# Performance work log

Measured on AMD Instinct MI355X. Metric: run time of the kernel, lower is better.

Reference implementation:

```python
import jax, jax.numpy as jnp
import numpy as np

D = 512       # d_model
M = 64        # working memory_dim
SE = 32       # episodic slots
SS = 64       # semantic slots
H = 4         # episodic heads
B, L = 2, 1024
BOT = max(D // 4, 32)  # controller bottleneck = 128


def _layernorm(x, g, b, eps=1e-5):
    mu = jnp.mean(x, axis=-1, keepdims=True)
    var = jnp.var(x, axis=-1, keepdims=True)
    return (x - mu) * jax.lax.rsqrt(var + eps) * g + b


def setup_inputs() -> dict:
    key = jax.random.key(0)
    ks = jax.random.split(key, 24)
    r = lambda i, shape, s=0.02: jax.random.normal(ks[i], shape, dtype=jnp.float32) * s
    return {
        "x": jax.random.normal(ks[0], (B, L, D), dtype=jnp.float32),
        # WorkingMemory (weights stored as (in, out))
        "Wq": r(1, (D, M)), "Wk": r(2, (D, M)), "Wv": r(3, (D, D)),
        "Wf": r(4, (D, M)), "bf": jnp.zeros((M,), jnp.float32),
        "Wo": r(5, (D, D)),
        "ln_g": jnp.ones((D,), jnp.float32), "ln_b": jnp.zeros((D,), jnp.float32),
        # EpisodicMemory
        "eslots": r(6, (1, SE, D)),
        "Eq": r(7, (D, D)), "Ek": r(8, (D, D)), "Ev": r(9, (D, D)), "Eo": r(10, (D, D)),
        # SemanticMemory
        "know": r(11, (1, SS, D)),
        "Sin": r(12, (D, D)),
        "Sg_w": r(13, (D, D)), "Sg_b": jnp.zeros((D,), jnp.float32),
        "So": r(14, (D, D)),
        # MemoryController
        "C1w": r(15, (D, BOT)), "C1b": jnp.zeros((BOT,), jnp.float32),
        "C2w": r(16, (BOT, 3)), "C2b": jnp.zeros((3,), jnp.float32),
    }


def _forward(x, Wq, Wk, Wv, Wf, bf, Wo, ln_g, ln_b,
             eslots, Eq, Ek, Ev, Eo,
             know, Sin, Sg_w, Sg_b, So,
             C1w, C1b, C2w, C2b):
    b, l, d = x.shape
    # ---- WorkingMemory (parallel gated linear attention) ----
    scale = M ** -0.5
    q = (jax.nn.elu(x @ Wq) + 1.0) * scale          # (B,L,M)
    k = jax.nn.elu(x @ Wk) + 1.0                    # (B,L,M)
    v = x @ Wv                                      # (B,L,D)
    forget = jax.nn.sigmoid(x @ Wf + bf)            # (B,L,M)
    log_f_cum = jnp.clip(jnp.cumsum(jnp.log(jnp.clip(forget, 1e-6, None)), axis=1), -20.0, 20.0)
    exp_neg = jnp.exp(-log_f_cum)
    exp_pos = jnp.exp(log_f_cum)
    kv = k[..., :, None] * v[..., None, :]          # (B,L,M,D) outer product
    cum_kv = jnp.cumsum(exp_neg[..., None] * kv, axis=1)
    Mstate = exp_pos[..., None] * cum_kv            # (B,L,M,D)
    z = exp_pos * jnp.cumsum(exp_neg * k, axis=1)   # (B,L,M)
    num = jnp.einsum('blm,blmd->bld', q, Mstate)
    den = jnp.einsum('blm,blm->bl', q, z)[..., None] + 1e-6
    w_out = _layernorm(num / den, ln_g, ln_b) @ Wo  # (B,L,D)

    # ---- EpisodicMemory (cross-attn to learned slots) ----
    hd = D // H
    mem = jnp.broadcast_to(eslots, (b, SE, D))
    qh = (x @ Eq).reshape(b, l, H, hd)
    kh = (mem @ Ek).reshape(b, SE, H, hd)
    vh = (mem @ Ev).reshape(b, SE, H, hd)
    scores = jnp.einsum('blhe,bshe->bhls', qh, kh) / jnp.sqrt(jnp.float32(hd))
    attn = jax.nn.softmax(scores, axis=-1)
    e_out = jnp.einsum('bhls,bshe->blhe', attn, vh).reshape(b, l, D) @ Eo

    # ---- SemanticMemory (single-head attn to knowledge, gated residual) ----
    kb = jnp.broadcast_to(know, (b, SS, D))
    qs = x @ Sin                                    # (B,L,D)
    s_scores = jnp.einsum('bld,bsd->bls', qs, kb) / jnp.sqrt(jnp.float32(D))
    s_attn = jax.nn.softmax(s_scores, axis=-1)
    retrieved = jnp.einsum('bls,bsd->bld', s_attn, kb)
    gate = jax.nn.sigmoid(x @ Sg_w + Sg_b)
    s_out = (gate * retrieved + (1.0 - gate) * x) @ So

    # ---- Controller fusion ----
    wts = jax.nn.softmax(jax.nn.silu(x @ C1w + C1b) @ C2w + C2b, axis=-1)  # (B,L,3)
    fused = (wts[..., 0:1] * w_out + wts[..., 1:2] * e_out + wts[..., 2:3] * s_out)
    return fused


def reference(x, Wq, Wk, Wv, Wf, bf, Wo, ln_g, ln_b,
              eslots, Eq, Ek, Ev, Eo,
              know, Sin, Sg_w, Sg_b, So,
              C1w, C1b, C2w, C2b):
    return _forward(x, Wq, Wk, Wv, Wf, bf, Wo, ln_g, ln_b,
                    eslots, Eq, Ek, Ev, Eo,
                    know, Sin, Sg_w, Sg_b, So,
                    C1w, C1b, C2w, C2b)
```

## Files before the change

### kernel.cpp

```cpp
#include <hip/hip_runtime.h>
#include <cstdint>

typedef unsigned int uint;
typedef unsigned short ushort;
typedef __attribute__((ext_vector_type(8))) short bf16x8;
typedef __attribute__((ext_vector_type(4))) float f32x4;

__device__ __forceinline__ ushort f2b(float f) {
  union { float f; uint u; } v; v.f = f;
  uint u = v.u;
  uint r = (u + 0x7FFFu + ((u >> 16) & 1u)) >> 16;
  return (ushort)r;
}
__device__ __forceinline__ float b2f(ushort h) {
  union { uint u; float f; } v; v.u = ((uint)h) << 16; return v.f;
}

__global__ __launch_bounds__(256) void k_prep(
    const float* __restrict__ x, const float* __restrict__ Wv, const float* __restrict__ Sg,
    const float* __restrict__ C1w, const float* __restrict__ Wq, const float* __restrict__ Wk,
    const float* __restrict__ Wo, const float* __restrict__ So, const float* __restrict__ know,
    const float* __restrict__ eslots, const float* __restrict__ Ek, const float* __restrict__ Ev,
    const float* __restrict__ Sin, const float* __restrict__ Wf, const float* __restrict__ bfb,
    ushort* __restrict__ X16, ushort* __restrict__ Wcat, ushort* __restrict__ Wfin,
    ushort* __restrict__ know16, float* __restrict__ kh, float* __restrict__ vh,
    float* __restrict__ logfb)
{
  __shared__ __align__(16) float pool[8320];
  int bid = blockIdx.x;
  int tid = threadIdx.x;
  int lane = tid & 63, wv = tid >> 6;

  if (bid < 128) {
    float* xS = pool;
    int r0 = bid * 16;
    #pragma unroll
    for (int it = 0; it < 8; ++it) {
      int p = it * 256 + tid;
      int rr = p >> 7, c4 = (p & 127) * 4;
      float4 v = *(const float4*)&x[(size_t)(r0 + rr) * 512 + c4];
      *(float4*)&xS[rr * 512 + c4] = v;
      uint2 o;
      o.x = (uint)f2b(v.x) | ((uint)f2b(v.y) << 16);
      o.y = (uint)f2b(v.z) | ((uint)f2b(v.w) << 16);
      *(uint2*)&X16[(size_t)(r0 + rr) * 512 + c4] = o;
    }
    __syncthreads();
    int row = tid >> 4, c4 = (tid & 15) * 4;
    float a0 = 0.f, a1 = 0.f, a2 = 0.f, a3 = 0.f;
    #pragma unroll 16
    for (int d = 0; d < 512; ++d) {
      float a = xS[row * 512 + d];
      float4 w = *(const float4*)&Wf[(size_t)d * 64 + c4];
      a0 += a * w.x; a1 += a * w.y; a2 += a * w.z; a3 += a * w.w;
    }
    float accs[4] = {a0, a1, a2, a3};
    #pragma unroll
    for (int j = 0; j < 4; ++j) {
      float logit = accs[j] + bfb[c4 + j];
      float s = 1.f / (1.f + expf(-logit));
      logfb[(size_t)(r0 + row) * 64 + c4 + j] = logf(fmaxf(s, 1e-6f));
    }
    return;
  }
  if (bid < 256) {
    int k = (bid - 128) * 4 + wv;
    const float* sp = Sin + (size_t)k * 512 + lane * 8;
    float4 s1 = *(const float4*)&sp[0];
    float4 s2 = *(const float4*)&sp[4];
    #pragma unroll 4
    for (int s = 0; s < 64; ++s) {
      const float* kp = know + (size_t)s * 512 + lane * 8;
      float4 k1 = *(const float4*)&kp[0];
      float4 k2 = *(const float4*)&kp[4];
      float part = s1.x * k1.x + s1.y * k1.y + s1.z * k1.z + s1.w * k1.w
                 + s2.x * k2.x + s2.y * k2.y + s2.z * k2.z + s2.w * k2.w;
      #pragma unroll
      for (int o = 32; o; o >>= 1) part += __shfl_xor(part, o);
      if (lane == 0) Wcat[(640 + s) * 512 + k] = f2b(part * 0.04419417382415922f);
    }
    return;
  }
  if (bid < 384) {
    int t = (bid - 256) * 256 + tid;
    int isv = (t >= 16384);
    int o = t & 16383; int s = o >> 9, j = o & 511;
    const float* W = isv ? Ev : Ek;
    const float* es = eslots + (size_t)s * 512;
    float a0 = 0.f, a1 = 0.f, a2 = 0.f, a3 = 0.f;
    #pragma unroll 8
    for (int d = 0; d < 512; d += 4) {
      a0 += es[d + 0] * W[(size_t)(d + 0) * 512 + j];
      a1 += es[d + 1] * W[(size_t)(d + 1) * 512 + j];
      a2 += es[d + 2] * W[(size_t)(d + 2) * 512 + j];
      a3 += es[d + 3] * W[(size_t)(d + 3) * 512 + j];
    }
    float acc = (a0 + a1) + (a2 + a3);
    (isv ? vh : kh)[(size_t)s * 512 + j] = acc;
    return;
  }
  if (bid < 672) {
    #define Tm(a,b) pool[(a) * 65 + (b)]
    int tt = bid - 384;
    const float* src; ushort* dst; int sld, dld, Nt, drow, dcol;
    if (tt < 64)       {           src = Wv;  dst = Wcat; sld = 512; dld = 512;  Nt = 8; drow = 0;    dcol = 0;   }
    else if (tt < 128) { tt -= 64; src = Sg;  dst = Wcat; sld = 512; dld = 512;  Nt = 8; drow = 704;  dcol = 0;   }
    else if (tt < 144) { tt -= 128; src = C1w; dst = Wcat; sld = 128; dld = 512; Nt = 2; drow = 1216; dcol = 0;   }
    else if (tt < 152) { tt -= 144; src = Wq;  dst = Wcat; sld = 64;  dld = 512; Nt = 1; drow = 1344; dcol = 0;   }
    else if (tt < 160) { tt -= 152; src = Wk;  dst = Wcat; sld = 64;  dld = 512; Nt = 1; drow = 1408; dcol = 0;   }
    else if (tt < 224) { tt -= 160; src = Wo;  dst = Wfin; sld = 512; dld = 1152; Nt = 8; drow = 0;   dcol = 0;   }
    else               { tt -= 224; src = So;  dst = Wfin; sld = 512; dld = 1152; Nt = 8; drow = 0;   dcol = 512; }
    int tk = tt / Nt, tn = tt % Nt;
    int k0 = tk * 64, n0 = tn * 64;
    int r = tid >> 4, c = (tid & 15) * 4;
    #pragma unroll
    for (int p = 0; p < 4; ++p) {
      int kk = p * 16 + r;
      float4 v = *(const float4*)&src[(size_t)(k0 + kk) * sld + n0 + c];
      Tm(c + 0, kk) = v.x; Tm(c + 1, kk) = v.y; Tm(c + 2, kk) = v.z; Tm(c + 3, kk) = v.w;
    }
    __syncthreads();
    int n = tid >> 2, kc = (tid & 3) * 16;
    uint u[8];
    #pragma unroll
    for (int j = 0; j < 8; ++j) {
      ushort lo = f2b(Tm(n, kc + 2 * j));
      ushort hi = f2b(Tm(n, kc + 2 * j + 1));
      u[j] = (uint)lo | ((uint)hi << 16);
    }
    size_t off = (size_t)(drow + n0 + n) * dld + dcol + k0 + kc;
    uint4 o1; o1.x = u[0]; o1.y = u[1]; o1.z = u[2]; o1.w = u[3];
    uint4 o2; o2.x = u[4]; o2.y = u[5]; o2.z = u[6]; o2.w = u[7];
    *(uint4*)&dst[off] = o1;
    *(uint4*)&dst[off + 8] = o2;
    #undef Tm
    return;
  }
  {
    int t = (bid - 672) * 256 + tid;
    #pragma unroll
    for (int j = 0; j < 2; ++j) {
      float4 v = *(const float4*)&know[(size_t)t * 8 + j * 4];
      uint2 o;
      o.x = (uint)f2b(v.x) | ((uint)f2b(v.y) << 16);
      o.y = (uint)f2b(v.z) | ((uint)f2b(v.w) << 16);
      *(uint2*)&know16[(size_t)t * 8 + j * 4] = o;
    }
  }
}

__global__ __launch_bounds__(256) void k_pre2(
    const float* __restrict__ Eq, const float* __restrict__ kh, const float* __restrict__ vh,
    const float* __restrict__ Eo, ushort* __restrict__ Wcat, ushort* __restrict__ Wfin)
{
  int bid = blockIdx.x;
  int tid = threadIdx.x;
  int lane = tid & 63, wv = tid >> 6;
  if (bid < 256) {
    int gw = bid * 4 + wv;
    #pragma unroll
    for (int pp = 0; pp < 2; ++pp) {
      int pair = gw * 2 + pp;
      int k = pair >> 2, h = pair & 3;
      const float* ep = Eq + (size_t)k * 512 + h * 128 + lane * 2;
      float e0 = ep[0], e1 = ep[1];
      #pragma unroll 4
      for (int s = 0; s < 32; ++s) {
        const float* kp = kh + (size_t)s * 512 + h * 128 + lane * 2;
        float part = e0 * kp[0] + e1 * kp[1];
        #pragma unroll
        for (int o = 32; o; o >>= 1) part += __shfl_xor(part, o);
        if (lane == 0) Wcat[(512 + h * 32 + s) * 512 + k] = f2b(part * 0.08838834764831845f);
      }
    }
  } else {
    int o = (bid - 256) * 256 + tid;
    int hs = o >> 9, j = o & 511;
    int h = hs >> 5, s = hs & 31;
    const float* vhp = vh + (size_t)s * 512 + h * 128;
    float acc = 0.f;
    #pragma unroll 16
    for (int e = 0; e < 128; ++e) acc += vhp[e] * Eo[(size_t)(h * 128 + e) * 512 + j];
    Wfin[(size_t)j * 1152 + 1024 + hs] = f2b(acc);
  }
}

__global__ __launch_bounds__(256) void k_gemm1(
    const ushort* __restrict__ A, const ushort* __restrict__ Bw, float* __restrict__ C,
    const float* __restrict__ sgb, const float* __restrict__ c1b)
{
  __shared__ __align__(16) ushort As[64 * 32];
  __shared__ __align__(16) ushort Bs[128 * 32];
  int tid = threadIdx.x;
  int lane = tid & 63, wv = tid >> 6;
  int wm = (wv & 1) * 32, wn = (wv >> 1) * 64;
  int lr = lane & 15, lk = lane >> 4;
  int m0 = blockIdx.y * 64, n0 = blockIdx.x * 128;
  f32x4 zero4 = {0.f, 0.f, 0.f, 0.f};
  f32x4 acc[2][4];
  #pragma unroll
  for (int a = 0; a < 2; ++a)
    #pragma unroll
    for (int b = 0; b < 4; ++b) acc[a][b] = zero4;
  for (int kt = 0; kt < 16; ++kt) {
    int k0 = kt * 32;
    {
      int p = tid, row = p >> 2, cc = p & 3;
      int cs = cc ^ ((row >> 1) & 3);
      *(uint4*)&As[p * 8] = *(const uint4*)&A[(size_t)(m0 + row) * 512 + k0 + cs * 8];
    }
    #pragma unroll
    for (int i = 0; i < 2; ++i) {
      int p = i * 256 + tid, row = p >> 2, cc = p & 3;
      int cs = cc ^ ((row >> 1) & 3);
      *(uint4*)&Bs[p * 8] = *(const uint4*)&Bw[(size_t)(n0 + row) * 512 + k0 + cs * 8];
    }
    __syncthreads();
    bf16x8 af[2], bfv[4];
    #pragma unroll
    for (int mi = 0; mi < 2; ++mi) {
      int row = wm + mi * 16 + lr;
      int cc = lk ^ ((row >> 1) & 3);
      af[mi] = *(bf16x8*)&As[row * 32 + cc * 8];
    }
    #pragma unroll
    for (int ni = 0; ni < 4; ++ni) {
      int row = wn + ni * 16 + lr;
      int cc = lk ^ ((row >> 1) & 3);
      bfv[ni] = *(bf16x8*)&Bs[row * 32 + cc * 8];
    }
    #pragma unroll
    for (int mi = 0; mi < 2; ++mi)
      #pragma unroll
      for (int ni = 0; ni < 4; ++ni)
        acc[mi][ni] = __builtin_amdgcn_mfma_f32_16x16x32_bf16(af[mi], bfv[ni], acc[mi][ni], 0, 0, 0);
    __syncthreads();
  }
  #pragma unroll
  for (int mi = 0; mi < 2; ++mi) {
    #pragma unroll
    for (int ni = 0; ni < 4; ++ni) {
      int col = n0 + wn + ni * 16 + lr;
      #pragma unroll
      for (int r = 0; r < 4; ++r) {
        int rowb = m0 + wm + mi * 16 + lk * 4 + r;
        float v = acc[mi][ni][r];
        if (col >= 704) {
          if (col < 1216) { v = 1.f / (1.f + __expf(-(v + sgb[col - 704]))); }
          else if (col < 1344) { float tt = v + c1b[col - 1216]; v = tt / (1.f + __expf(-tt)); }
          else if (col < 1408) { float e = (v > 0.f) ? v : (__expf(v) - 1.f); v = (e + 1.f) * 0.125f; }
          else if (col < 1472) { float e = (v > 0.f) ? v : (__expf(v) - 1.f); v = e + 1.f; }
        }
        C[(size_t)rowb * 1536 + col] = v;
      }
    }
  }
}

__global__ __launch_bounds__(256) void k_gemm2(
    const ushort* __restrict__ A, const ushort* __restrict__ Bw, float* __restrict__ C)
{
  __shared__ __align__(16) ushort As[64 * 32];
  __shared__ __align__(16) ushort Bs[64 * 32];
  int tid = threadIdx.x;
  int lane = tid & 63, wv = tid >> 6;
  int wm = (wv & 1) * 32, wn = (wv >> 1) * 32;
  int lr = lane & 15, lk = lane >> 4;
  int m0 = blockIdx.y * 64, n0 = blockIdx.x * 64;
  f32x4 zero4 = {0.f, 0.f, 0.f, 0.f};
  f32x4 acc[2][2];
  #pragma unroll
  for (int a = 0; a < 2; ++a)
    #pragma unroll
    for (int b = 0; b < 2; ++b) acc[a][b] = zero4;
  for (int kt = 0; kt < 36; ++kt) {
    int k0 = kt * 32;
    {
      int p = tid, row = p >> 2, cc = p & 3;
      int cs = cc ^ ((row >> 1) & 3);
      *(uint4*)&As[p * 8] = *(const uint4*)&A[(size_t)(m0 + row) * 1152 + k0 + cs * 8];
      *(uint4*)&Bs[p * 8] = *(const uint4*)&Bw[(size_t)(n0 + row) * 1152 + k0 + cs * 8];
    }
    __syncthreads();
    bf16x8 af[2], bfv[2];
    #pragma unroll
    for (int mi = 0; mi < 2; ++mi) {
      int row = wm + mi * 16 + lr;
      int cc = lk ^ ((row >> 1) & 3);
      af[mi] = *(bf16x8*)&As[row * 32 + cc * 8];
    }
    #pragma unroll
    for (int ni = 0; ni < 2; ++ni) {
      int row = wn + ni * 16 + lr;
      int cc = lk ^ ((row >> 1) & 3);
      bfv[ni] = *(bf16x8*)&Bs[row * 32 + cc * 8];
    }
    #pragma unroll
    for (int mi = 0; mi < 2; ++mi)
      #pragma unroll
      for (int ni = 0; ni < 2; ++ni)
        acc[mi][ni] = __builtin_amdgcn_mfma_f32_16x16x32_bf16(af[mi], bfv[ni], acc[mi][ni], 0, 0, 0);
    __syncthreads();
  }
  #pragma unroll
  for (int mi = 0; mi < 2; ++mi) {
    #pragma unroll
    for (int ni = 0; ni < 2; ++ni) {
      int col = n0 + wn + ni * 16 + lr;
      #pragma unroll
      for (int r = 0; r < 4; ++r) {
        int rowb = m0 + wm + mi * 16 + lk * 4 + r;
        C[(size_t)rowb * 512 + col] = acc[mi][ni][r];
      }
    }
  }
}

__global__ __launch_bounds__(256) void k_gatescan(
    const float* __restrict__ logfb, const float* __restrict__ P,
    float* __restrict__ cn, float* __restrict__ qe, float* __restrict__ qz)
{
  __shared__ float wsumA[4];
  __shared__ float wsumB[4];
  int bidx = blockIdx.x;
  int b = bidx >> 6, m = bidx & 63;
  int tid = threadIdx.x;
  int lane = tid & 63, wv = tid >> 6;
  size_t rbase = (size_t)b * 1024 + tid * 4;

  float v0 = logfb[(rbase + 0) * 64 + m];
  float v1 = logfb[(rbase + 1) * 64 + m];
  float v2 = logfb[(rbase + 2) * 64 + m];
  float v3 = logfb[(rbase + 3) * 64 + m];
  v1 += v0; v2 += v1; v3 += v2;
  float tsum = v3;
  float sc = tsum;
  #pragma unroll
  for (int o = 1; o < 64; o <<= 1) {
    float t = __shfl_up(sc, o, 64);
    if (lane >= o) sc += t;
  }
  if (lane == 63) wsumA[wv] = sc;
  __syncthreads();
  float excl = sc - tsum;
  #pragma unroll
  for (int w2 = 0; w2 < 3; ++w2) if (w2 < wv) excl += wsumA[w2];

  float vv[4] = {v0, v1, v2, v3};
  float cv[4], qv[4];
  #pragma unroll
  for (int i = 0; i < 4; ++i) {
    size_t r = rbase + i;
    float lf = fminf(fmaxf(excl + vv[i], -20.f), 20.f);
    float en = expf(-lf), ep = expf(lf);
    float kk = P[r * 1536 + 1408 + m];
    float qq = P[r * 1536 + 1344 + m];
    cv[i] = en * kk;
    qv[i] = qq * ep;
    cn[r * 64 + m] = cv[i];
    qe[r * 64 + m] = qv[i];
  }

  float c1 = cv[0], c2 = c1 + cv[1], c3 = c2 + cv[2], c4 = c3 + cv[3];
  float t2 = c4;
  float sc2 = t2;
  #pragma unroll
  for (int o = 1; o < 64; o <<= 1) {
    float t = __shfl_up(sc2, o, 64);
    if (lane >= o) sc2 += t;
  }
  if (lane == 63) wsumB[wv] = sc2;
  __syncthreads();
  float excl2 = sc2 - t2;
  #pragma unroll
  for (int w2 = 0; w2 < 3; ++w2) if (w2 < wv) excl2 += wsumB[w2];

  float pr[4] = {c1, c2, c3, c4};
  #pragma unroll
  for (int i = 0; i < 4; ++i) {
    size_t r = rbase + i;
    qz[r * 64 + m] = qv[i] * (excl2 + pr[i]);
  }
}

__global__ __launch_bounds__(256) void k_scanA(
    const float* __restrict__ cn, const float* __restrict__ P, float* __restrict__ Send)
{
  __shared__ __align__(16) float cnS[32 * 64];
  __shared__ __align__(16) float vS[16 * 64];
  int tid = threadIdx.x;
  int bid = blockIdx.x;
  int dt = bid & 7, c = (bid >> 3) & 31, b = bid >> 8;
  int rb0 = b * 1024 + c * 32;
  #pragma unroll
  for (int it = 0; it < 2; ++it) {
    int p = it * 256 + tid;
    int row = p >> 4, c4f = (p & 15) * 4;
    *(float4*)&cnS[row * 64 + c4f] = *(const float4*)&cn[(size_t)(rb0 + row) * 64 + c4f];
  }
  __syncthreads();
  int mg = tid >> 4, dl = tid & 15;
  float4 acc[4];
  #pragma unroll
  for (int i = 0; i < 4; ++i) acc[i] = make_float4(0.f, 0.f, 0.f, 0.f);
  for (int ig = 0; ig < 2; ++ig) {
    int rb = rb0 + ig * 16;
    int row = tid >> 4, c4f = (tid & 15) * 4;
    *(float4*)&vS[row * 64 + c4f] = *(const float4*)&P[(size_t)(rb + row) * 1536 + dt * 64 + c4f];
    __syncthreads();
    #pragma unroll 4
    for (int i = 0; i < 16; ++i) {
      float4 vv = *(float4*)&vS[i * 64 + dl * 4];
      float4 cm = *(float4*)&cnS[(ig * 16 + i) * 64 + mg * 4];
      acc[0].x += cm.x * vv.x; acc[0].y += cm.x * vv.y; acc[0].z += cm.x * vv.z; acc[0].w += cm.x * vv.w;
      acc[1].x += cm.y * vv.x; acc[1].y += cm.y * vv.y; acc[1].z += cm.y * vv.z; acc[1].w += cm.y * vv.w;
      acc[2].x += cm.z * vv.x; acc[2].y += cm.z * vv.y; acc[2].z += cm.z * vv.z; acc[2].w += cm.z * vv.w;
      acc[3].x += cm.w * vv.x; acc[3].y += cm.w * vv.y; acc[3].z += cm.w * vv.z; acc[3].w += cm.w * vv.w;
    }
    __syncthreads();
  }
  #pragma unroll
  for (int mi = 0; mi < 4; ++mi) {
    int m = mg * 4 + mi;
    *(float4*)&Send[(size_t)((b * 32 + c) * 64 + m) * 512 + dt * 64 + dl * 4] = acc[mi];
  }
}

__global__ __launch_bounds__(256) void k_scanB(const float* __restrict__ Send, float* __restrict__ carry)
{
  int t = blockIdx.x * 256 + threadIdx.x;
  int d = t & 511, m = (t >> 9) & 63, b = t >> 15;
  float run = 0.f;
  #pragma unroll 8
  for (int c = 0; c < 32; ++c) {
    size_t idx = (size_t)((b * 32 + c) * 64 + m) * 512 + d;
    carry[idx] = run;
    run += Send[idx];
  }
}

__global__ __launch_bounds__(256) void k_scanC(
    const float* __restrict__ cn, const float* __restrict__ qe, const float* __restrict__ P,
    const float* __restrict__ carry, float* __restrict__ num)
{
  __shared__ __align__(16) float cnS[32 * 64];
  __shared__ __align__(16) float qeS[32 * 64];
  __shared__ __align__(16) float vS[16 * 64];
  int tid = threadIdx.x;
  int bid = blockIdx.x;
  int dt = bid & 7, c = (bid >> 3) & 31, b = bid >> 8;
  int rb0 = b * 1024 + c * 32;
  #pragma unroll
  for (int it = 0; it < 2; ++it) {
    int p = it * 256 + tid;
    int row = p >> 4, c4f = (p & 15) * 4;
    *(float4*)&cnS[row * 64 + c4f] = *(const float4*)&cn[(size_t)(rb0 + row) * 64 + c4f];
    *(float4*)&qeS[row * 64 + c4f] = *(const float4*)&qe[(size_t)(rb0 + row) * 64 + c4f];
  }
  int mg = tid & 3, dl = tid >> 2;
  int d = dt * 64 + dl;
  float S[16];
  #pragma unroll
  for (int mi = 0; mi < 16; ++mi)
    S[mi] = carry[(size_t)((b * 32 + c) * 64 + mg * 16 + mi) * 512 + d];
  __syncthreads();
  for (int ig = 0; ig < 2; ++ig) {
    int rb = rb0 + ig * 16;
    int row = tid >> 4, c4f = (tid & 15) * 4;
    *(float4*)&vS[row * 64 + c4f] = *(const float4*)&P[(size_t)(rb + row) * 1536 + dt * 64 + c4f];
    __syncthreads();
    for (int i = 0; i < 16; ++i) {
      int ii = ig * 16 + i;
      float vv = vS[i * 64 + dl];
      float p = 0.f;
      #pragma unroll
      for (int j = 0; j < 4; ++j) {
        float4 c4 = *(float4*)&cnS[ii * 64 + mg * 16 + j * 4];
        float4 q4 = *(float4*)&qeS[ii * 64 + mg * 16 + j * 4];
        S[j * 4 + 0] += c4.x * vv; p += q4.x * S[j * 4 + 0];
        S[j * 4 + 1] += c4.y * vv; p += q4.y * S[j * 4 + 1];
        S[j * 4 + 2] += c4.z * vv; p += q4.z * S[j * 4 + 2];
        S[j * 4 + 3] += c4.w * vv; p += q4.w * S[j * 4 + 3];
      }
      p += __shfl_xor(p, 1);
      p += __shfl_xor(p, 2);
      if (mg == 0) num[(size_t)(rb0 + ii) * 512 + d] = p;
    }
    __syncthreads();
  }
}

__global__ __launch_bounds__(256) void k_post(
    const float* __restrict__ P, const float* __restrict__ x,
    const float* __restrict__ num, const float* __restrict__ qz,
    const ushort* __restrict__ know16, const float* __restrict__ lng,
    const float* __restrict__ lnb, const float* __restrict__ C2w,
    const float* __restrict__ C2b, ushort* __restrict__ Afin)
{
  __shared__ __align__(16) ushort kbuf[32 * 512];
  __shared__ float attnL[4][64];
  __shared__ float w2L[4];
  int tid = threadIdx.x;
  int w = tid >> 6, lane = tid & 63;
  int r0 = blockIdx.x * 4;
  int r = r0 + w;
  size_t pr = (size_t)r * 1536;

  float h0 = P[pr + 1216 + lane], h1 = P[pr + 1280 + lane];
  float a0 = h0 * C2w[lane * 3 + 0] + h1 * C2w[(64 + lane) * 3 + 0];
  float a1 = h0 * C2w[lane * 3 + 1] + h1 * C2w[(64 + lane) * 3 + 1];
  float a2 = h0 * C2w[lane * 3 + 2] + h1 * C2w[(64 + lane) * 3 + 2];
  #pragma unroll
  for (int o = 32; o; o >>= 1) {
    a0 += __shfl_xor(a0, o); a1 += __shfl_xor(a1, o); a2 += __shfl_xor(a2, o);
  }
  a0 += C2b[0]; a1 += C2b[1]; a2 += C2b[2];
  float mxc = fmaxf(a0, fmaxf(a1, a2));
  float e0 = expf(a0 - mxc), e1 = expf(a1 - mxc), e2c = expf(a2 - mxc);
  float inv = 1.f / (e0 + e1 + e2c);
  float w0 = e0 * inv, w1 = e1 * inv, w2 = e2c * inv;
  if (lane == 0) w2L[w] = w2;

  {
    float den = qz[(size_t)r * 64 + lane];
    #pragma unroll
    for (int o = 32; o; o >>= 1) den += __shfl_xor(den, o);
    den += 1e-6f;
    float y[8];
    float4 n0 = *(const float4*)&num[(size_t)r * 512 + lane * 8];
    float4 n1 = *(const float4*)&num[(size_t)r * 512 + lane * 8 + 4];
    y[0] = n0.x / den; y[1] = n0.y / den; y[2] = n0.z / den; y[3] = n0.w / den;
    y[4] = n1.x / den; y[5] = n1.y / den; y[6] = n1.z / den; y[7] = n1.w / den;
    float s1 = 0.f, s2 = 0.f;
    #pragma unroll
    for (int i = 0; i < 8; ++i) { s1 += y[i]; s2 += y[i] * y[i]; }
    #pragma unroll
    for (int o = 32; o; o >>= 1) { s1 += __shfl_xor(s1, o); s2 += __shfl_xor(s2, o); }
    float mu = s1 * (1.f / 512.f);
    float var = s2 * (1.f / 512.f) - mu * mu;
    float rs = rsqrtf(var + 1e-5f);
    uint4 outv;
    uint pk[4];
    #pragma unroll
    for (int p2 = 0; p2 < 4; ++p2) {
      float o0 = (y[2 * p2] - mu) * rs * lng[lane * 8 + 2 * p2] + lnb[lane * 8 + 2 * p2];
      float o1 = (y[2 * p2 + 1] - mu) * rs * lng[lane * 8 + 2 * p2 + 1] + lnb[lane * 8 + 2 * p2 + 1];
      pk[p2] = (uint)f2b(o0 * w0) | ((uint)f2b(o1 * w0) << 16);
    }
    outv.x = pk[0]; outv.y = pk[1]; outv.z = pk[2]; outv.w = pk[3];
    *(uint4*)&Afin[(size_t)r * 1152 + lane * 8] = outv;
  }

  {
    int h = lane >> 4, ei = (lane & 15) * 2;
    float v0 = P[pr + 512 + h * 32 + ei], v1 = P[pr + 512 + h * 32 + ei + 1];
    float mxe = fmaxf(v0, v1);
    #pragma unroll
    for (int o = 1; o < 16; o <<= 1) mxe = fmaxf(mxe, __shfl_xor(mxe, o));
    float ee0 = __expf(v0 - mxe), ee1 = __expf(v1 - mxe);
    float ss = ee0 + ee1;
    #pragma unroll
    for (int o = 1; o < 16; o <<= 1) ss += __shfl_xor(ss, o);
    float sc1 = w1 / ss;
    uint pkv = (uint)f2b(ee0 * sc1) | ((uint)f2b(ee1 * sc1) << 16);
    *(uint*)&Afin[(size_t)r * 1152 + 1024 + h * 32 + ei] = pkv;
  }

  {
    float lv = P[pr + 640 + lane];
    float mx = lv;
    #pragma unroll
    for (int o = 32; o; o >>= 1) mx = fmaxf(mx, __shfl_xor(mx, o));
    float e = __expf(lv - mx);
    float sum = e;
    #pragma unroll
    for (int o = 32; o; o >>= 1) sum += __shfl_xor(sum, o);
    attnL[w][lane] = e / sum;
  }
  __syncthreads();

  int dd = tid * 2;
  float acc[4][2];
  #pragma unroll
  for (int i = 0; i < 4; ++i) { acc[i][0] = 0.f; acc[i][1] = 0.f; }
  for (int hs = 0; hs < 2; ++hs) {
    #pragma unroll
    for (int i = 0; i < 8; ++i) {
      int idx = i * 256 + tid;
      *(uint4*)&kbuf[idx * 8] = *(const uint4*)&know16[(size_t)hs * 16384 + idx * 8];
    }
    __syncthreads();
    for (int s = 0; s < 32; ++s) {
      uint uu = *(uint*)&kbuf[s * 512 + dd];
      float k0 = b2f((ushort)(uu & 0xffff));
      float k1 = b2f((ushort)(uu >> 16));
      #pragma unroll
      for (int row = 0; row < 4; ++row) {
        float a = attnL[row][hs * 32 + s];
        acc[row][0] += a * k0;
        acc[row][1] += a * k1;
      }
    }
    __syncthreads();
  }
  #pragma unroll
  for (int row = 0; row < 4; ++row) {
    int rr = r0 + row;
    float g0 = P[(size_t)rr * 1536 + 704 + dd];
    float g1 = P[(size_t)rr * 1536 + 704 + dd + 1];
    float x0 = x[(size_t)rr * 512 + dd], x1 = x[(size_t)rr * 512 + dd + 1];
    float w2v = w2L[row];
    float m0 = g0 * acc[row][0] + (1.f - g0) * x0;
    float m1 = g1 * acc[row][1] + (1.f - g1) * x1;
    uint pkv = (uint)f2b(w2v * m0) | ((uint)f2b(w2v * m1) << 16);
    *(uint*)&Afin[(size_t)rr * 1152 + 512 + dd] = pkv;
  }
}

extern "C" void kernel_launch(void* const* d_in, const int* in_sizes, int n_in,
                              void* d_out, int out_size, void* d_ws, size_t ws_size,
                              hipStream_t stream)
{
  const float* x     = (const float*)d_in[0];
  const float* Wq    = (const float*)d_in[1];
  const float* Wk    = (const float*)d_in[2];
  const float* Wv    = (const float*)d_in[3];
  const float* Wf    = (const float*)d_in[4];
  const float* bfb   = (const float*)d_in[5];
  const float* Wo    = (const float*)d_in[6];
  const float* ln_g  = (const float*)d_in[7];
  const float* ln_b  = (const float*)d_in[8];
  const float* eslots= (const float*)d_in[9];
  const float* Eq    = (const float*)d_in[10];
  const float* Ek    = (const float*)d_in[11];
  const float* Ev    = (const float*)d_in[12];
  const float* Eo    = (const float*)d_in[13];
  const float* know  = (const float*)d_in[14];
  const float* Sin   = (const float*)d_in[15];
  const float* Sg_w  = (const float*)d_in[16];
  const float* Sg_b  = (const float*)d_in[17];
  const float* So    = (const float*)d_in[18];
  const float* C1w   = (const float*)d_in[19];
  const float* C1b   = (const float*)d_in[20];
  const float* C2w   = (const float*)d_in[21];
  const float* C2b   = (const float*)d_in[22];

  char* ws = (char*)d_ws;
  ushort* X16    = (ushort*)(ws + 0);
  ushort* Wcat   = (ushort*)(ws + 2097152);
  ushort* Wfin   = (ushort*)(ws + 3670016);
  ushort* know16 = (ushort*)(ws + 4849664);
  float*  kh     = (float*)(ws + 4915200);
  float*  vh     = (float*)(ws + 4980736);
  float*  P      = (float*)(ws + 5046272);
  float*  logfb  = (float*)(ws + 17629184);
  float*  cn     = (float*)(ws + 18153472);
  float*  qe     = (float*)(ws + 18677760);
  float*  qz     = (float*)(ws + 19202048);
  float*  Send   = (float*)(ws + 19726336);
  float*  carry  = (float*)(ws + 28114944);
  float*  num    = (float*)(ws + 36503552);
  ushort* Afin   = (ushort*)(ws + 40697856);

  k_prep<<<dim3(688), dim3(256), 0, stream>>>(x, Wv, Sg_w, C1w, Wq, Wk, Wo, So, know,
                                              eslots, Ek, Ev, Sin, Wf, bfb,
                                              X16, Wcat, Wfin, know16, kh, vh, logfb);
  k_pre2<<<dim3(512), dim3(256), 0, stream>>>(Eq, kh, vh, Eo, Wcat, Wfin);
  k_gemm1<<<dim3(12, 32), dim3(256), 0, stream>>>(X16, Wcat, P, Sg_b, C1b);
  k_gatescan<<<dim3(128), dim3(256), 0, stream>>>(logfb, P, cn, qe, qz);
  k_scanA<<<dim3(512), dim3(256), 0, stream>>>(cn, P, Send);
  k_scanB<<<dim3(256), dim3(256), 0, stream>>>(Send, carry);
  k_scanC<<<dim3(512), dim3(256), 0, stream>>>(cn, qe, P, carry, num);
  k_post<<<dim3(512), dim3(256), 0, stream>>>(P, x, num, qz, know16, ln_g, ln_b, C2w, C2b, Afin);
  k_gemm2<<<dim3(8, 32), dim3(256), 0, stream>>>(Afin, Wfin, (float*)d_out);
}
```

Measured before the change: 139.2 us.

## Tile eslots projection via LDS and move off-critical-path prep into mid kernel

Rewrites the eslots×Ek/Ev projection so each block stages 32-row weight tiles in shared memory and computes four slots per thread, cutting redundant global reads of the weight matrices. The vh×Eo fold into Wfin and the know→bf16 conversion move out of the pre-GEMM kernels into the gate-scan kernel, which runs after gemm1, so they fill otherwise idle CUs during the small scan launch and shorten the critical path before gemm1. The tiled projection uses fewer blocks (16), which may limit parallelism for that piece.

```diff
diff --git a/kernel.cpp b/kernel.cpp
--- a/kernel.cpp
+++ b/kernel.cpp
@@ -23,8 +23,7 @@
     const float* __restrict__ eslots, const float* __restrict__ Ek, const float* __restrict__ Ev,
     const float* __restrict__ Sin, const float* __restrict__ Wf, const float* __restrict__ bfb,
     ushort* __restrict__ X16, ushort* __restrict__ Wcat, ushort* __restrict__ Wfin,
-    ushort* __restrict__ know16, float* __restrict__ kh, float* __restrict__ vh,
-    float* __restrict__ logfb)
+    float* __restrict__ kh, float* __restrict__ vh, float* __restrict__ logfb)
 {
   __shared__ __align__(16) float pool[8320];
   int bid = blockIdx.x;
@@ -81,27 +80,42 @@
     }
     return;
   }
-  if (bid < 384) {
-    int t = (bid - 256) * 256 + tid;
-    int isv = (t >= 16384);
-    int o = t & 16383; int s = o >> 9, j = o & 511;
+  if (bid < 272) {
+    float* Wt = pool;
+    int b2 = bid - 256;
+    int isv = b2 >= 8;
+    int jb = (b2 & 7) * 64;
     const float* W = isv ? Ev : Ek;
-    const float* es = eslots + (size_t)s * 512;
-    float a0 = 0.f, a1 = 0.f, a2 = 0.f, a3 = 0.f;
-    #pragma unroll 8
-    for (int d = 0; d < 512; d += 4) {
-      a0 += es[d + 0] * W[(size_t)(d + 0) * 512 + j];
-      a1 += es[d + 1] * W[(size_t)(d + 1) * 512 + j];
-      a2 += es[d + 2] * W[(size_t)(d + 2) * 512 + j];
-      a3 += es[d + 3] * W[(size_t)(d + 3) * 512 + j];
-    }
-    float acc = (a0 + a1) + (a2 + a3);
-    (isv ? vh : kh)[(size_t)s * 512 + j] = acc;
+    float* out = isv ? vh : kh;
+    int jl = tid & 63, sg = tid >> 6;
+    float acc[4] = {0.f, 0.f, 0.f, 0.f};
+    for (int dc = 0; dc < 16; ++dc) {
+      #pragma unroll
+      for (int it = 0; it < 2; ++it) {
+        int p = it * 256 + tid;
+        int row = p >> 4, c4 = (p & 15) * 4;
+        *(float4*)&Wt[row * 64 + c4] = *(const float4*)&W[(size_t)(dc * 32 + row) * 512 + jb + c4];
+      }
+      __syncthreads();
+      #pragma unroll 8
+      for (int d2 = 0; d2 < 32; ++d2) {
+        float wval = Wt[d2 * 64 + jl];
+        int d = dc * 32 + d2;
+        acc[0] += eslots[(size_t)(sg * 4 + 0) * 512 + d] * wval;
+        acc[1] += eslots[(size_t)(sg * 4 + 1) * 512 + d] * wval;
+        acc[2] += eslots[(size_t)(sg * 4 + 2) * 512 + d] * wval;
+        acc[3] += eslots[(size_t)(sg * 4 + 3) * 512 + d] * wval;
+      }
+      __syncthreads();
+    }
+    #pragma unroll
+    for (int si = 0; si < 4; ++si)
+      out[(size_t)(sg * 4 + si) * 512 + jb + jl] = acc[si];
     return;
   }
-  if (bid < 672) {
+  {
     #define Tm(a,b) pool[(a) * 65 + (b)]
-    int tt = bid - 384;
+    int tt = bid - 272;
     const float* src; ushort* dst; int sld, dld, Nt, drow, dcol;
     if (tt < 64)       {           src = Wv;  dst = Wcat; sld = 512; dld = 512;  Nt = 8; drow = 0;    dcol = 0;   }
     else if (tt < 128) { tt -= 64; src = Sg;  dst = Wcat; sld = 512; dld = 512;  Nt = 8; drow = 704;  dcol = 0;   }
@@ -134,54 +148,30 @@
     *(uint4*)&dst[off] = o1;
     *(uint4*)&dst[off + 8] = o2;
     #undef Tm
-    return;
-  }
-  {
-    int t = (bid - 672) * 256 + tid;
-    #pragma unroll
-    for (int j = 0; j < 2; ++j) {
-      float4 v = *(const float4*)&know[(size_t)t * 8 + j * 4];
-      uint2 o;
-      o.x = (uint)f2b(v.x) | ((uint)f2b(v.y) << 16);
-      o.y = (uint)f2b(v.z) | ((uint)f2b(v.w) << 16);
-      *(uint2*)&know16[(size_t)t * 8 + j * 4] = o;
-    }
   }
 }
 
 __global__ __launch_bounds__(256) void k_pre2(
-    const float* __restrict__ Eq, const float* __restrict__ kh, const float* __restrict__ vh,
-    const float* __restrict__ Eo, ushort* __restrict__ Wcat, ushort* __restrict__ Wfin)
+    const float* __restrict__ Eq, const float* __restrict__ kh, ushort* __restrict__ Wcat)
 {
   int bid = blockIdx.x;
   int tid = threadIdx.x;
   int lane = tid & 63, wv = tid >> 6;
-  if (bid < 256) {
-    int gw = bid * 4 + wv;
-    #pragma unroll
-    for (int pp = 0; pp < 2; ++pp) {
-      int pair = gw * 2 + pp;
-      int k = pair >> 2, h = pair & 3;
-      const float* ep = Eq + (size_t)k * 512 + h * 128 + lane * 2;
-      float e0 = ep[0], e1 = ep[1];
-      #pragma unroll 4
-      for (int s = 0; s < 32; ++s) {
-        const float* kp = kh + (size_t)s * 512 + h * 128 + lane * 2;
-        float part = e0 * kp[0] + e1 * kp[1];
-        #pragma unroll
-        for (int o = 32; o; o >>= 1) part += __shfl_xor(part, o);
-        if (lane == 0) Wcat[(512 + h * 32 + s) * 512 + k] = f2b(part * 0.08838834764831845f);
-      }
-    }
-  } else {
-    int o = (bid - 256) * 256 + tid;
-    int hs = o >> 9, j = o & 511;
-    int h = hs >> 5, s = hs & 31;
-    const float* vhp = vh + (size_t)s * 512 + h * 128;
-    float acc = 0.f;
-    #pragma unroll 16
-    for (int e = 0; e < 128; ++e) acc += vhp[e] * Eo[(size_t)(h * 128 + e) * 512 + j];
-    Wfin[(size_t)j * 1152 + 1024 + hs] = f2b(acc);
+  int gw = bid * 4 + wv;
+  #pragma unroll
+  for (int pp = 0; pp < 2; ++pp) {
+    int pair = gw * 2 + pp;
+    int k = pair >> 2, h = pair & 3;
+    const float* ep = Eq + (size_t)k * 512 + h * 128 + lane * 2;
+    float e0 = ep[0], e1 = ep[1];
+    #pragma unroll 4
+    for (int s = 0; s < 32; ++s) {
+      const float* kp = kh + (size_t)s * 512 + h * 128 + lane * 2;
+      float part = e0 * kp[0] + e1 * kp[1];
+      #pragma unroll
+      for (int o = 32; o; o >>= 1) part += __shfl_xor(part, o);
+      if (lane == 0) Wcat[(512 + h * 32 + s) * 512 + k] = f2b(part * 0.08838834764831845f);
+    }
   }
 }
 
@@ -316,70 +306,97 @@
   }
 }
 
-__global__ __launch_bounds__(256) void k_gatescan(
+__global__ __launch_bounds__(256) void k_mid(
     const float* __restrict__ logfb, const float* __restrict__ P,
-    float* __restrict__ cn, float* __restrict__ qe, float* __restrict__ qz)
+    float* __restrict__ cn, float* __restrict__ qe, float* __restrict__ qz,
+    const float* __restrict__ vh, const float* __restrict__ Eo, ushort* __restrict__ Wfin,
+    const float* __restrict__ know, ushort* __restrict__ know16)
 {
   __shared__ float wsumA[4];
   __shared__ float wsumB[4];
-  int bidx = blockIdx.x;
-  int b = bidx >> 6, m = bidx & 63;
-  int tid = threadIdx.x;
-  int lane = tid & 63, wv = tid >> 6;
-  size_t rbase = (size_t)b * 1024 + tid * 4;
-
-  float v0 = logfb[(rbase + 0) * 64 + m];
-  float v1 = logfb[(rbase + 1) * 64 + m];
-  float v2 = logfb[(rbase + 2) * 64 + m];
-  float v3 = logfb[(rbase + 3) * 64 + m];
-  v1 += v0; v2 += v1; v3 += v2;
-  float tsum = v3;
-  float sc = tsum;
-  #pragma unroll
-  for (int o = 1; o < 64; o <<= 1) {
-    float t = __shfl_up(sc, o, 64);
-    if (lane >= o) sc += t;
-  }
-  if (lane == 63) wsumA[wv] = sc;
-  __syncthreads();
-  float excl = sc - tsum;
-  #pragma unroll
-  for (int w2 = 0; w2 < 3; ++w2) if (w2 < wv) excl += wsumA[w2];
-
-  float vv[4] = {v0, v1, v2, v3};
-  float cv[4], qv[4];
-  #pragma unroll
-  for (int i = 0; i < 4; ++i) {
-    size_t r = rbase + i;
-    float lf = fminf(fmaxf(excl + vv[i], -20.f), 20.f);
-    float en = expf(-lf), ep = expf(lf);
-    float kk = P[r * 1536 + 1408 + m];
-    float qq = P[r * 1536 + 1344 + m];
-    cv[i] = en * kk;
-    qv[i] = qq * ep;
-    cn[r * 64 + m] = cv[i];
-    qe[r * 64 + m] = qv[i];
-  }
-
-  float c1 = cv[0], c2 = c1 + cv[1], c3 = c2 + cv[2], c4 = c3 + cv[3];
-  float t2 = c4;
-  float sc2 = t2;
-  #pragma unroll
-  for (int o = 1; o < 64; o <<= 1) {
-    float t = __shfl_up(sc2, o, 64);
-    if (lane >= o) sc2 += t;
-  }
-  if (lane == 63) wsumB[wv] = sc2;
-  __syncthreads();
-  float excl2 = sc2 - t2;
-  #pragma unroll
-  for (int w2 = 0; w2 < 3; ++w2) if (w2 < wv) excl2 += wsumB[w2];
-
-  float pr[4] = {c1, c2, c3, c4};
-  #pragma unroll
-  for (int i = 0; i < 4; ++i) {
-    size_t r = rbase + i;
-    qz[r * 64 + m] = qv[i] * (excl2 + pr[i]);
+  int bid = blockIdx.x;
+  int tid = threadIdx.x;
+  if (bid < 128) {
+    int b = bid >> 6, m = bid & 63;
+    int lane = tid & 63, wv = tid >> 6;
+    size_t rbase = (size_t)b * 1024 + tid * 4;
+
+    float v0 = logfb[(rbase + 0) * 64 + m];
+    float v1 = logfb[(rbase + 1) * 64 + m];
+    float v2 = logfb[(rbase + 2) * 64 + m];
+    float v3 = logfb[(rbase + 3) * 64 + m];
+    v1 += v0; v2 += v1; v3 += v2;
+    float tsum = v3;
+    float sc = tsum;
+    #pragma unroll
+    for (int o = 1; o < 64; o <<= 1) {
+      float t = __shfl_up(sc, o, 64);
+      if (lane >= o) sc += t;
+    }
+    if (lane == 63) wsumA[wv] = sc;
+    __syncthreads();
+    float excl = sc - tsum;
+    #pragma unroll
+    for (int w2 = 0; w2 < 3; ++w2) if (w2 < wv) excl += wsumA[w2];
+
+    float vv[4] = {v0, v1, v2, v3};
+    float cv[4], qv[4];
+    #pragma unroll
+    for (int i = 0; i < 4; ++i) {
+      size_t r = rbase + i;
+      float lf = fminf(fmaxf(excl + vv[i], -20.f), 20.f);
+      float en = expf(-lf), ep = expf(lf);
+      float kk = P[r * 1536 + 1408 + m];
+      float qq = P[r * 1536 + 1344 + m];
+      cv[i] = en * kk;
+      qv[i] = qq * ep;
+      cn[r * 64 + m] = cv[i];
+      qe[r * 64 + m] = qv[i];
+    }
+
+    float c1 = cv[0], c2 = c1 + cv[1], c3 = c2 + cv[2], c4 = c3 + cv[3];
+    float t2 = c4;
+    float sc2 = t2;
+    #pragma unroll
+    for (int o = 1; o < 64; o <<= 1) {
+      float t = __shfl_up(sc2, o, 64);
+      if (lane >= o) sc2 += t;
+    }
+    if (lane == 63) wsumB[wv] = sc2;
+    __syncthreads();
+    float excl2 = sc2 - t2;
+    #pragma unroll
+    for (int w2 = 0; w2 < 3; ++w2) if (w2 < wv) excl2 += wsumB[w2];
+
+    float pr[4] = {c1, c2, c3, c4};
+    #pragma unroll
+    for (int i = 0; i < 4; ++i) {
+      size_t r = rbase + i;
+      qz[r * 64 + m] = qv[i] * (excl2 + pr[i]);
+    }
+    return;
+  }
+  if (bid < 384) {
+    int o = (bid - 128) * 256 + tid;
+    int hs = o >> 9, j = o & 511;
+    int h = hs >> 5, s = hs & 31;
+    const float* vhp = vh + (size_t)s * 512 + h * 128;
+    float acc = 0.f;
+    #pragma unroll 16
+    for (int e = 0; e < 128; ++e) acc += vhp[e] * Eo[(size_t)(h * 128 + e) * 512 + j];
+    Wfin[(size_t)j * 1152 + 1024 + hs] = f2b(acc);
+    return;
+  }
+  {
+    int t = (bid - 384) * 256 + tid;
+    #pragma unroll
+    for (int j = 0; j < 2; ++j) {
+      float4 v = *(const float4*)&know[(size_t)t * 8 + j * 4];
+      uint2 o;
+      o.x = (uint)f2b(v.x) | ((uint)f2b(v.y) << 16);
+      o.y = (uint)f2b(v.z) | ((uint)f2b(v.w) << 16);
+      *(uint2*)&know16[(size_t)t * 8 + j * 4] = o;
+    }
   }
 }
 
@@ -662,12 +679,12 @@
   float*  num    = (float*)(ws + 36503552);
   ushort* Afin   = (ushort*)(ws + 40697856);
 
-  k_prep<<<dim3(688), dim3(256), 0, stream>>>(x, Wv, Sg_w, C1w, Wq, Wk, Wo, So, know,
+  k_prep<<<dim3(560), dim3(256), 0, stream>>>(x, Wv, Sg_w, C1w, Wq, Wk, Wo, So, know,
                                               eslots, Ek, Ev, Sin, Wf, bfb,
-                                              X16, Wcat, Wfin, know16, kh, vh, logfb);
-  k_pre2<<<dim3(512), dim3(256), 0, stream>>>(Eq, kh, vh, Eo, Wcat, Wfin);
+                                              X16, Wcat, Wfin, kh, vh, logfb);
+  k_pre2<<<dim3(256), dim3(256), 0, stream>>>(Eq, kh, Wcat);
   k_gemm1<<<dim3(12, 32), dim3(256), 0, stream>>>(X16, Wcat, P, Sg_b, C1b);
-  k_gatescan<<<dim3(128), dim3(256), 0, stream>>>(logfb, P, cn, qe, qz);
+  k_mid<<<dim3(400), dim3(256), 0, stream>>>(logfb, P, cn, qe, qz, vh, Eo, Wfin, know, know16);
   k_scanA<<<dim3(512), dim3(256), 0, stream>>>(cn, P, Send);
   k_scanB<<<dim3(256), dim3(256), 0, stream>>>(Send, carry);
   k_scanC<<<dim3(512), dim3(256), 0, stream>>>(cn, qe, P, carry, num);
```

Result: slower. 151.0 us (+8.5%).
